# Performance work log

Hardware: AMD Instinct MI355X
Metric: run time of the kernel (lower is better)

The kernel has to match this reference:

```python
import jax, jax.numpy as jnp
import numpy as np

HEADS = 16

def setup_inputs() -> dict:
    key = jax.random.key(0)
    ks = jax.random.split(key, 4)
    emb = 1024
    x = jax.random.normal(ks[0], (2, 2048, emb), dtype=jnp.float32)
    Wqkv = jax.random.normal(ks[1], (emb, 3 * emb), dtype=jnp.float32) * 0.02
    bqkv = jnp.zeros((3 * emb,), dtype=jnp.float32)
    Wproj = jax.random.normal(ks[2], (emb, emb), dtype=jnp.float32) * 0.02
    bproj = jnp.zeros((emb,), dtype=jnp.float32)
    return {"x": x, "Wqkv": Wqkv, "bqkv": bqkv, "Wproj": Wproj, "bproj": bproj}


def reference(x, Wqkv, bqkv, Wproj, bproj):
    b, n, e = x.shape
    h = HEADS
    d = e // h
    # qkv projection; last dim factors as (h, d, 3): q/k/v interleaved innermost,
    # matching einops rearrange 'b n (h d q) -> q b h n d'
    t = (x @ Wqkv + bqkv).reshape(b, n, h, d, 3)
    q, k, v = t[..., 0], t[..., 1], t[..., 2]  # each [b, n, h, d]
    scale = np.float32(1.0 / np.sqrt(e))  # note: sqrt(emb), not sqrt(head_dim)
    att = jax.nn.softmax(jnp.einsum('bnhd,bmhd->bhnm', q, k) * scale, axis=-1)
    out = jnp.einsum('bhnm,bmhd->bnhd', att, v).reshape(b, n, e)
    return out @ Wproj + bproj
```

## Files before the change

### kernel.cpp

```cpp
#include <hip/hip_runtime.h>

typedef __bf16 bf16;
typedef __attribute__((ext_vector_type(8))) __bf16 bf16x8;
typedef __attribute__((ext_vector_type(4))) float f32x4;
typedef __attribute__((ext_vector_type(16))) float f32x16;
typedef unsigned int u32;
typedef __attribute__((ext_vector_type(2))) unsigned int u32x2;
typedef __attribute__((ext_vector_type(4))) unsigned int u32x4;

#define SEQ 2048
#define EMB 1024
#define NH  16
#define DH  64


__global__ __launch_bounds__(256) void conv_f32_bf16(const float* __restrict__ in,
                                                     bf16* __restrict__ out, int n8) {
    int i = blockIdx.x * blockDim.x + threadIdx.x;
    if (i >= n8) return;
    float4 a = ((const float4*)in)[2 * i];
    float4 b = ((const float4*)in)[2 * i + 1];
    bf16x8 o;
    o[0] = (bf16)a.x; o[1] = (bf16)a.y; o[2] = (bf16)a.z; o[3] = (bf16)a.w;
    o[4] = (bf16)b.x; o[5] = (bf16)b.y; o[6] = (bf16)b.z; o[7] = (bf16)b.w;
    ((bf16x8*)out)[i] = o;
}

__global__ __launch_bounds__(256) void transpose_f32_bf16(const float* __restrict__ in,
                                                          bf16* __restrict__ out,
                                                          int R, int C) {
    __shared__ float t[32][33];
    int tx = threadIdx.x & 31, ty = threadIdx.x >> 5;
    int c0 = blockIdx.x * 32, r0 = blockIdx.y * 32;
#pragma unroll
    for (int s = 0; s < 4; s++) {
        int row = ty + s * 8;
        t[row][tx] = in[(size_t)(r0 + row) * C + c0 + tx];
    }
    __syncthreads();
#pragma unroll
    for (int s = 0; s < 4; s++) {
        int row = ty + s * 8;
        out[(size_t)(c0 + row) * R + r0 + tx] = (bf16)t[tx][row];
    }
}

__global__ __launch_bounds__(256) void transpose_permute_qkv(const float* __restrict__ in,
                                                             bf16* __restrict__ out) {
    __shared__ float t[32][33];
    int tx = threadIdx.x & 31, ty = threadIdx.x >> 5;
    int c0 = blockIdx.x * 32, r0 = blockIdx.y * 32;
#pragma unroll
    for (int s = 0; s < 4; s++) {
        int row = ty + s * 8;
        t[row][tx] = in[(size_t)(r0 + row) * 3072 + c0 + tx];
    }
    __syncthreads();
#pragma unroll
    for (int s = 0; s < 4; s++) {
        int row = ty + s * 8;
        int corig = c0 + row;
        int hh = corig / 192;
        int rem = corig - hh * 192;
        int dd = rem / 3;
        int which = rem - dd * 3;
        int colp = which * 1024 + hh * 64 + dd;
        out[(size_t)colp * EMB + r0 + tx] = (bf16)t[tx][row];
    }
}


#define BM 128
#define BN 128
#define BK 32

__device__ __forceinline__ void gload16(const bf16* g, bf16* l) {
    __builtin_amdgcn_global_load_lds((__attribute__((address_space(1))) void*)(void*)g,
                                     (__attribute__((address_space(3))) void*)l, 16, 0, 0);
}

__device__ __forceinline__ void stage_tile(const bf16* src, int ld, int row0, int k0,
                                           bf16* lds, int wave, int lane) {
#pragma unroll
    for (int c = 0; c < 2; c++) {
        int chunk = wave + 4 * c;
        int row = chunk * 16 + (lane >> 2);
        int slot = (lane & 3) ^ ((lane >> 2) & 3);
        const bf16* g = src + (size_t)(row0 + row) * ld + k0 + slot * 8;
        gload16(g, lds + chunk * 512);
    }
}

__device__ __forceinline__ bf16x8 frag(const bf16* lds, int row, int s) {
    int slot = s ^ (row & 3);
    return *(const bf16x8*)&lds[row * BK + slot * 8];
}

__device__ __forceinline__ void gemm_mainloop(const bf16* A, const bf16* Bt, int Kdim,
                                              int m0, int n0, bf16* As, bf16* Bs,
                                              int wave, int lane, int wr, int wc,
                                              f32x4 acc[4][4]) {
    stage_tile(A, Kdim, m0, 0, As, wave, lane);
    stage_tile(Bt, Kdim, n0, 0, Bs, wave, lane);
    asm volatile("s_waitcnt vmcnt(0)" ::: "memory");
    __builtin_amdgcn_s_barrier();

    int cur = 0;
    const int iters = Kdim / BK;
    for (int it = 0; it < iters; ++it) {
        if (it + 1 < iters) {
            stage_tile(A, Kdim, m0, (it + 1) * BK, As + (cur ^ 1) * BM * BK, wave, lane);
            stage_tile(Bt, Kdim, n0, (it + 1) * BK, Bs + (cur ^ 1) * BN * BK, wave, lane);
        }
        const bf16* as = As + cur * BM * BK;
        const bf16* bs = Bs + cur * BN * BK;
        int s = lane >> 4;
        bf16x8 a[4], b[4];
#pragma unroll
        for (int i = 0; i < 4; i++)
            a[i] = frag(as, wr * 64 + i * 16 + (lane & 15), s);
#pragma unroll
        for (int j = 0; j < 4; j++)
            b[j] = frag(bs, wc * 64 + j * 16 + (lane & 15), s);
#pragma unroll
        for (int i = 0; i < 4; i++)
#pragma unroll
            for (int j = 0; j < 4; j++)
                acc[i][j] = __builtin_amdgcn_mfma_f32_16x16x32_bf16(a[i], b[j], acc[i][j], 0, 0, 0);
        asm volatile("s_waitcnt vmcnt(0)" ::: "memory");
        __builtin_amdgcn_s_barrier();
        cur ^= 1;
    }
}

__global__ __launch_bounds__(256) void gemm_qkv(const bf16* __restrict__ A,
                                                const bf16* __restrict__ Bt,
                                                const float* __restrict__ bias,
                                                bf16* __restrict__ Qb, bf16* __restrict__ Kb,
                                                bf16* __restrict__ Vt) {
    __shared__ alignas(16) bf16 smem[4 * BM * BK];
    bf16* As = smem;
    bf16* Bs = smem + 2 * BM * BK;
    int wave = threadIdx.x >> 6, lane = threadIdx.x & 63;
    int wr = wave >> 1, wc = wave & 1;

    int flat = blockIdx.y * 24 + blockIdx.x;
    int swz = (flat & 7) * 96 + (flat >> 3);
    int n0 = (swz % 24) * BN;
    int m0 = (swz / 24) * BM;

    f32x4 acc[4][4] = {};
    gemm_mainloop(A, Bt, EMB, m0, n0, As, Bs, wave, lane, wr, wc, acc);

    int which = n0 >> 10;
    bool isV = (which == 2);
    char* tile = (char*)smem;

#pragma unroll
    for (int i = 0; i < 4; i++) {
#pragma unroll
        for (int j = 0; j < 4; j++) {
            int c = wc * 64 + j * 16 + (lane & 15);
            int hh = ((n0 + c) >> 6) & 15;
            int dd = c & 63;
            float bv = bias[hh * 192 + dd * 3 + which];
#pragma unroll
            for (int r = 0; r < 4; r++) {
                int rowL = wr * 64 + i * 16 + 4 * (lane >> 4) + r;
                float v = acc[i][j][r] + bv;
                if (which == 0) v *= 0.03125f;
                int byte;
                if (!isV) byte = rowL * 256 + ((c * 2) ^ ((rowL & 7) << 4));
                else      byte = c * 256 + ((((rowL >> 3) ^ (c & 15)) << 4) + (rowL & 7) * 2);
                *(bf16*)(tile + byte) = (bf16)v;
            }
        }
    }
    __builtin_amdgcn_s_barrier();

    int tid = threadIdx.x;
    if (which == 0) {
#pragma unroll
        for (int k = 0; k < 8; k++) {
            int f = k * 256 + tid;
            int rowL = f >> 4, ch = f & 15;
            bf16x8 val = *(const bf16x8*)(tile + rowL * 256 + ((ch ^ (rowL & 7)) << 4));
            int grow = m0 + rowL;
            int bb = grow >> 11, npos = grow & 2047;
            int cbase = ch * 8;
            int hh = ((n0 + cbase) >> 6) & 15;
            int d0 = cbase & 63;
            *(bf16x8*)(Qb + (((size_t)bb * NH + hh) * SEQ + npos) * DH + d0) = val;
        }
    } else if (which == 1) {
#pragma unroll
        for (int k = 0; k < 8; k++) {
            int f = k * 256 + tid;
            int rowL = f >> 4, ch = f & 15;
            bf16x8 val = *(const bf16x8*)(tile + rowL * 256 + ((ch ^ (rowL & 7)) << 4));
            int grow = m0 + rowL;
            int bb = grow >> 11, npos = grow & 2047;
            int cbase = ch * 8;
            int hh = ((n0 + cbase) >> 6) & 15;
            int d0 = cbase & 63;
            size_t base = ((size_t)bb * NH + hh) * (SEQ * DH) + (size_t)(npos >> 6) * 4096;
            int chunk = ((npos >> 5) & 1) * 8 + (d0 >> 4) * 2 + ((d0 >> 3) & 1);
            *(bf16x8*)(Kb + base + chunk * 256 + (npos & 31) * 8) = val;
        }
    } else {
#pragma unroll
        for (int k = 0; k < 8; k++) {
            int f = k * 256 + tid;
            int cL = f >> 4, g = f & 15;
            bf16x8 val = *(const bf16x8*)(tile + cL * 256 + ((g ^ (cL & 15)) << 4));
            int grow = m0 + g * 8;
            int bb = grow >> 11, nn = grow & 2047;
            int hh = ((n0 + cL) >> 6) & 15;
            int d = cL & 63;
            int tIdx = nn >> 6;
            int mb = nn & 63;
            int mc = mb >> 4, half = (mb >> 3) & 1;
            char* base = (char*)Vt +
                         (((size_t)bb * NH + hh) * (SEQ * DH) + (size_t)tIdx * 4096) * 2;
            u32x4 vv = __builtin_bit_cast(u32x4, val);
            u32x2 lo = {vv.x, vv.y};
            u32x2 hi = {vv.z, vv.w};
            int off = ((d >> 5) * 4 + mc) * 1024 + (d & 31) * 16 + half * 8;
            *(u32x2*)(base + off) = lo;
            *(u32x2*)(base + off + 512) = hi;
        }
    }
}

__global__ __launch_bounds__(256) void gemm_proj(const bf16* __restrict__ A,
                                                 const bf16* __restrict__ Bt,
                                                 const float* __restrict__ bias,
                                                 float* __restrict__ C) {
    __shared__ alignas(16) bf16 smem[4 * BM * BK];
    bf16* As = smem;
    bf16* Bs = smem + 2 * BM * BK;
    int wave = threadIdx.x >> 6, lane = threadIdx.x & 63;
    int wr = wave >> 1, wc = wave & 1;
    int m0 = blockIdx.y * BM, n0 = blockIdx.x * BN;
    f32x4 acc[4][4] = {};
    gemm_mainloop(A, Bt, EMB, m0, n0, As, Bs, wave, lane, wr, wc, acc);

    int m_base = m0 + wr * 64;
    int n_base = n0 + wc * 64;
#pragma unroll
    for (int i = 0; i < 4; i++) {
#pragma unroll
        for (int j = 0; j < 4; j++) {
            int col = n_base + j * 16 + (lane & 15);
            float bv = bias[col];
#pragma unroll
            for (int r = 0; r < 4; r++) {
                int row = m_base + i * 16 + 4 * (lane >> 4) + r;
                C[(size_t)row * EMB + col] = acc[i][j][r] + bv;
            }
        }
    }
}


__device__ __forceinline__ void stage16k(const bf16* src, bf16* lds, int wave, int lane) {
#pragma unroll
    for (int i = 0; i < 4; i++) {
        int c = wave * 4 + i;
        gload16(src + c * 512 + lane * 8, lds + c * 512);
    }
}

__device__ __forceinline__ u32 pack_bf16(float lo, float hi) {
    unsigned short a = __builtin_bit_cast(unsigned short, (bf16)lo);
    unsigned short b = __builtin_bit_cast(unsigned short, (bf16)hi);
    return (u32)a | ((u32)b << 16);
}

__global__ __launch_bounds__(256, 2) void attn(const bf16* __restrict__ Q,
                                               const bf16* __restrict__ K,
                                               const bf16* __restrict__ Vt,
                                               bf16* __restrict__ O) {
    int flat = blockIdx.x;
    int swz = (flat & 7) * 64 + (flat >> 3);
    int bh = swz >> 4;
    int qb = swz & 15;

    int wave = threadIdx.x >> 6, lane = threadIdx.x & 63;
    int l31 = lane & 31, h = lane >> 5;
    int qw0 = qb * 128 + wave * 32;
    const bf16* Qg = Q + (size_t)bh * SEQ * DH;
    const bf16* Kg = K + (size_t)bh * SEQ * DH;
    const bf16* Vg = Vt + (size_t)bh * SEQ * DH;

    __shared__ alignas(16) bf16 Ks[2][8192];
    __shared__ alignas(16) bf16 Vs[2][8192];

    bf16x8 qf[4];
#pragma unroll
    for (int ks = 0; ks < 4; ks++)
        qf[ks] = *(const bf16x8*)(Qg + (size_t)(qw0 + l31) * DH + ks * 16 + h * 8);

    f32x16 Oc[2] = {};
    float lsum = 0.f;

    stage16k(Kg, &Ks[0][0], wave, lane);
    stage16k(Vg, &Vs[0][0], wave, lane);
    asm volatile("s_waitcnt vmcnt(0)" ::: "memory");
    __builtin_amdgcn_s_barrier();

    int cur = 0;
    const int NIT = SEQ / 128;
    for (int it = 0; it < NIT; ++it) {
        if (it + 1 < NIT) {
            stage16k(Kg + (size_t)(it + 1) * 8192, &Ks[cur ^ 1][0], wave, lane);
            stage16k(Vg + (size_t)(it + 1) * 8192, &Vs[cur ^ 1][0], wave, lane);
        }
        const char* kc = (const char*)&Ks[cur][0];
        const char* vc = (const char*)&Vs[cur][0];

        u32 w[4][8];
        float part[4];
#pragma unroll
        for (int T = 0; T < 4; T++) {
            bf16x8 kf[4];
#pragma unroll
            for (int ks = 0; ks < 4; ks++)
                kf[ks] = *(const bf16x8*)(kc + (((T * 4 + ks) * 2 + h) << 9) + l31 * 16);
            f32x16 st = {};
#pragma unroll
            for (int ks = 0; ks < 4; ks++)
                st = __builtin_amdgcn_mfma_f32_32x32x16_bf16(kf[ks], qf[ks], st, 0, 0, 0);
            float acc = 0.f;
#pragma unroll
            for (int p = 0; p < 8; p++) {
                float p0 = __expf(st[2 * p]);
                float p1 = __expf(st[2 * p + 1]);
                acc += p0 + p1;
                w[T][p] = pack_bf16(p0, p1);
            }
            part[T] = acc;
        }
        lsum += (part[0] + part[1]) + (part[2] + part[3]);

#pragma unroll
        for (int mg = 0; mg < 2; mg++)
#pragma unroll
            for (int dt = 0; dt < 2; dt++)
#pragma unroll
                for (int mc = 0; mc < 4; mc++) {
                    bf16x8 vf = *(const bf16x8*)(vc + mg * 8192 +
                                                 (((dt * 4 + mc) * 2 + h) << 9) + l31 * 16);
                    int Tw = mg * 2 + (mc >> 1);
                    u32x4 pw = {w[Tw][4 * (mc & 1) + 0], w[Tw][4 * (mc & 1) + 1],
                                w[Tw][4 * (mc & 1) + 2], w[Tw][4 * (mc & 1) + 3]};
                    bf16x8 pa = __builtin_bit_cast(bf16x8, pw);
                    Oc[dt] = __builtin_amdgcn_mfma_f32_32x32x16_bf16(pa, vf, Oc[dt], 0, 0, 0);
                }

        asm volatile("s_waitcnt vmcnt(0)" ::: "memory");
        __builtin_amdgcn_s_barrier();
        cur ^= 1;
    }

    float ls = lsum + __shfl_xor(lsum, 32);
    float rinv = 1.0f / ls;
    int bb = bh >> 4, hh = bh & 15;
#pragma unroll
    for (int reg = 0; reg < 16; reg++) {
        int qlocal = (reg & 3) + 8 * (reg >> 2) + 4 * h;
        float sc = __shfl(rinv, qlocal);
        int row = qw0 + qlocal;
#pragma unroll
        for (int dt = 0; dt < 2; dt++) {
            O[((size_t)bb * SEQ + row) * EMB + hh * DH + dt * 32 + l31] =
                (bf16)(Oc[dt][reg] * sc);
        }
    }
}


extern "C" void kernel_launch(void* const* d_in, const int* in_sizes, int n_in,
                              void* d_out, int out_size, void* d_ws, size_t ws_size,
                              hipStream_t stream) {
    const float* x     = (const float*)d_in[0];
    const float* Wqkv  = (const float*)d_in[1];
    const float* bqkv  = (const float*)d_in[2];
    const float* Wproj = (const float*)d_in[3];
    const float* bproj = (const float*)d_in[4];
    float* out = (float*)d_out;
    char* ws = (char*)d_ws;

    bf16* xb     = (bf16*)(ws + 0);
    bf16* attO   = xb;
    bf16* WqkvT  = (bf16*)(ws + 8388608);
    bf16* WprojT = (bf16*)(ws + 14680064);
    bf16* Qb     = (bf16*)(ws + 16777216);
    bf16* Kb     = (bf16*)(ws + 25165824);
    bf16* Vt     = (bf16*)(ws + 33554432);

    conv_f32_bf16<<<2048, 256, 0, stream>>>(x, xb, 524288);
    transpose_permute_qkv<<<dim3(96, 32), 256, 0, stream>>>(Wqkv, WqkvT);
    transpose_f32_bf16<<<dim3(32, 32), 256, 0, stream>>>(Wproj, WprojT, EMB, EMB);
    gemm_qkv<<<dim3(24, 32), 256, 0, stream>>>(xb, WqkvT, bqkv, Qb, Kb, Vt);
    attn<<<512, 256, 0, stream>>>(Qb, Kb, Vt, attO);
    gemm_proj<<<dim3(8, 32), 256, 0, stream>>>(attO, WprojT, bproj, out);
}
```

Before: 134.1 us.

## Merge prep kernels into one launch and read V directly from global in attention

The three conversion/transpose kernels are combined into a single prep kernel that dispatches on block index, which removes two kernel launches. The attention kernel no longer stages V tiles through LDS and instead loads V fragments straight from global memory, which halves the LDS footprint and may allow more resident blocks. The trade-off is that the V loads are now uncoalesced-ish per-lane 16-byte global reads in the MFMA inner loop, with their latency no longer hidden by the double-buffered prefetch.

Measured after the change: 133.2 us. About the same (-0.7%).

```diff
diff --git a/kernel.cpp b/kernel.cpp
--- a/kernel.cpp
+++ b/kernel.cpp
@@ -13,59 +13,56 @@
 #define NH  16
 #define DH  64
 
-
-__global__ __launch_bounds__(256) void conv_f32_bf16(const float* __restrict__ in,
-                                                     bf16* __restrict__ out, int n8) {
-    int i = blockIdx.x * blockDim.x + threadIdx.x;
-    if (i >= n8) return;
-    float4 a = ((const float4*)in)[2 * i];
-    float4 b = ((const float4*)in)[2 * i + 1];
-    bf16x8 o;
-    o[0] = (bf16)a.x; o[1] = (bf16)a.y; o[2] = (bf16)a.z; o[3] = (bf16)a.w;
-    o[4] = (bf16)b.x; o[5] = (bf16)b.y; o[6] = (bf16)b.z; o[7] = (bf16)b.w;
-    ((bf16x8*)out)[i] = o;
-}
-
-__global__ __launch_bounds__(256) void transpose_f32_bf16(const float* __restrict__ in,
-                                                          bf16* __restrict__ out,
-                                                          int R, int C) {
+__global__ __launch_bounds__(256) void prep(const float* __restrict__ x, bf16* __restrict__ xb,
+                                            const float* __restrict__ Wqkv, bf16* __restrict__ WqkvT,
+                                            const float* __restrict__ Wproj, bf16* __restrict__ WprojT) {
     __shared__ float t[32][33];
+    int b = blockIdx.x;
+    if (b < 2048) {
+        int i = b * 256 + threadIdx.x;
+        float4 a = ((const float4*)x)[2 * i];
+        float4 c = ((const float4*)x)[2 * i + 1];
+        bf16x8 o;
+        o[0] = (bf16)a.x; o[1] = (bf16)a.y; o[2] = (bf16)a.z; o[3] = (bf16)a.w;
+        o[4] = (bf16)c.x; o[5] = (bf16)c.y; o[6] = (bf16)c.z; o[7] = (bf16)c.w;
+        ((bf16x8*)xb)[i] = o;
+        return;
+    }
     int tx = threadIdx.x & 31, ty = threadIdx.x >> 5;
-    int c0 = blockIdx.x * 32, r0 = blockIdx.y * 32;
-#pragma unroll
-    for (int s = 0; s < 4; s++) {
-        int row = ty + s * 8;
-        t[row][tx] = in[(size_t)(r0 + row) * C + c0 + tx];
-    }
-    __syncthreads();
-#pragma unroll
-    for (int s = 0; s < 4; s++) {
-        int row = ty + s * 8;
-        out[(size_t)(c0 + row) * R + r0 + tx] = (bf16)t[tx][row];
-    }
-}
-
-__global__ __launch_bounds__(256) void transpose_permute_qkv(const float* __restrict__ in,
-                                                             bf16* __restrict__ out) {
-    __shared__ float t[32][33];
-    int tx = threadIdx.x & 31, ty = threadIdx.x >> 5;
-    int c0 = blockIdx.x * 32, r0 = blockIdx.y * 32;
-#pragma unroll
-    for (int s = 0; s < 4; s++) {
-        int row = ty + s * 8;
-        t[row][tx] = in[(size_t)(r0 + row) * 3072 + c0 + tx];
-    }
-    __syncthreads();
-#pragma unroll
-    for (int s = 0; s < 4; s++) {
-        int row = ty + s * 8;
-        int corig = c0 + row;
-        int hh = corig / 192;
-        int rem = corig - hh * 192;
-        int dd = rem / 3;
-        int which = rem - dd * 3;
-        int colp = which * 1024 + hh * 64 + dd;
-        out[(size_t)colp * EMB + r0 + tx] = (bf16)t[tx][row];
+    if (b < 5120) {
+        int flat = b - 2048;
+        int c0 = (flat % 96) * 32, r0 = (flat / 96) * 32;
+#pragma unroll
+        for (int s = 0; s < 4; s++) {
+            int row = ty + s * 8;
+            t[row][tx] = Wqkv[(size_t)(r0 + row) * 3072 + c0 + tx];
+        }
+        __syncthreads();
+#pragma unroll
+        for (int s = 0; s < 4; s++) {
+            int row = ty + s * 8;
+            int corig = c0 + row;
+            int hh = corig / 192;
+            int rem = corig - hh * 192;
+            int dd = rem / 3;
+            int which = rem - dd * 3;
+            int colp = which * 1024 + hh * 64 + dd;
+            WqkvT[(size_t)colp * EMB + r0 + tx] = (bf16)t[tx][row];
+        }
+    } else {
+        int flat = b - 5120;
+        int c0 = (flat % 32) * 32, r0 = (flat / 32) * 32;
+#pragma unroll
+        for (int s = 0; s < 4; s++) {
+            int row = ty + s * 8;
+            t[row][tx] = Wproj[(size_t)(r0 + row) * EMB + c0 + tx];
+        }
+        __syncthreads();
+#pragma unroll
+        for (int s = 0; s < 4; s++) {
+            int row = ty + s * 8;
+            WprojT[(size_t)(c0 + row) * EMB + r0 + tx] = (bf16)t[tx][row];
+        }
     }
 }
 
@@ -294,7 +291,6 @@
     const bf16* Vg = Vt + (size_t)bh * SEQ * DH;
 
     __shared__ alignas(16) bf16 Ks[2][8192];
-    __shared__ alignas(16) bf16 Vs[2][8192];
 
     bf16x8 qf[4];
 #pragma unroll
@@ -305,7 +301,6 @@
     float lsum = 0.f;
 
     stage16k(Kg, &Ks[0][0], wave, lane);
-    stage16k(Vg, &Vs[0][0], wave, lane);
     asm volatile("s_waitcnt vmcnt(0)" ::: "memory");
     __builtin_amdgcn_s_barrier();
 
@@ -314,10 +309,9 @@
     for (int it = 0; it < NIT; ++it) {
         if (it + 1 < NIT) {
             stage16k(Kg + (size_t)(it + 1) * 8192, &Ks[cur ^ 1][0], wave, lane);
-            stage16k(Vg + (size_t)(it + 1) * 8192, &Vs[cur ^ 1][0], wave, lane);
         }
         const char* kc = (const char*)&Ks[cur][0];
-        const char* vc = (const char*)&Vs[cur][0];
+        const bf16* vgi = Vg + (size_t)it * 8192;
 
         u32 w[4][8];
         float part[4];
@@ -349,8 +343,8 @@
             for (int dt = 0; dt < 2; dt++)
 #pragma unroll
                 for (int mc = 0; mc < 4; mc++) {
-                    bf16x8 vf = *(const bf16x8*)(vc + mg * 8192 +
-                                                 (((dt * 4 + mc) * 2 + h) << 9) + l31 * 16);
+                    bf16x8 vf = *(const bf16x8*)(vgi + mg * 4096 +
+                                                 ((dt * 4 + mc) * 2 + h) * 256 + l31 * 8);
                     int Tw = mg * 2 + (mc >> 1);
                     u32x4 pw = {w[Tw][4 * (mc & 1) + 0], w[Tw][4 * (mc & 1) + 1],
                                 w[Tw][4 * (mc & 1) + 2], w[Tw][4 * (mc & 1) + 3]};
@@ -399,9 +393,7 @@
     bf16* Kb     = (bf16*)(ws + 25165824);
     bf16* Vt     = (bf16*)(ws + 33554432);
 
-    conv_f32_bf16<<<2048, 256, 0, stream>>>(x, xb, 524288);
-    transpose_permute_qkv<<<dim3(96, 32), 256, 0, stream>>>(Wqkv, WqkvT);
-    transpose_f32_bf16<<<dim3(32, 32), 256, 0, stream>>>(Wproj, WprojT, EMB, EMB);
+    prep<<<6144, 256, 0, stream>>>(x, xb, Wqkv, WqkvT, Wproj, WprojT);
     gemm_qkv<<<dim3(24, 32), 256, 0, stream>>>(xb, WqkvT, bqkv, Qb, Kb, Vt);
     attn<<<512, 256, 0, stream>>>(Qb, Kb, Vt, attO);
     gemm_proj<<<dim3(8, 32), 256, 0, stream>>>(attO, WprojT, bproj, out);
```
